# Kernel optimization log

Measured on AMD Instinct MI355X. Metric: run time of the kernel, lower is better.

The kernel has to match this reference:

```python
import jax, jax.numpy as jnp
import numpy as np

N = 80000    # total nodes
E = 640000   # total edges
B = 800      # graphs in batch
NPG = 100    # nodes per graph
HID = 128
NC = 10
IND = 20     # one-hot degree feature size (torch.eye(20))
EPS = 1e-5


def _gconv(x, src, dst, inv_out, inv_in, W, b):
    # DGL GraphConv, norm='both': D_out^{-1/2} scaling at src, sum-aggregate, D_in^{-1/2} at dst
    m = (x * inv_out[:, None])[src]                      # [E, F]
    agg = jax.ops.segment_sum(m, dst, num_segments=x.shape[0])
    return (agg * inv_in[:, None]) @ W + b


def _bn(x, gamma, beta):
    # BatchNorm1d, training-mode (batch statistics, biased variance)
    mu = x.mean(0)
    var = x.var(0)
    return (x - mu) / jnp.sqrt(var + EPS) * gamma + beta


def setup_inputs():
    key = jax.random.key(0)
    ks = jax.random.split(key, 10)
    # edges constrained within each graph (batched disjoint graphs, as in dgl.batch)
    eg = jax.random.randint(ks[0], (E,), 0, B)
    src = (eg * NPG + jax.random.randint(ks[1], (E,), 0, NPG)).astype(jnp.int32)
    dst = (eg * NPG + jax.random.randint(ks[2], (E,), 0, NPG)).astype(jnp.int32)
    graph_id = (jnp.arange(N) // NPG).astype(jnp.int32)

    def p(k, shape, fan):
        return (jax.random.normal(k, shape, jnp.float32) / np.sqrt(fan)).astype(jnp.float32)

    z = lambda s: jnp.zeros(s, jnp.float32)
    o = lambda s: jnp.ones(s, jnp.float32)
    return dict(
        src=src, dst=dst, graph_id=graph_id,
        W1=p(ks[3], (IND, HID), IND), b1=z((HID,)), g1=o((HID,)), be1=z((HID,)),
        W2=p(ks[4], (HID, HID), HID), b2=z((HID,)), g2=o((HID,)), be2=z((HID,)),
        Wv=p(ks[5], (HID, 1), HID), bv=z((1,)),
        Wd=p(ks[6], (1, HID), 1), bd=z((HID,)),
        Wg=p(ks[7], (HID, HID), HID), bg=z((HID,)), g3=o((HID,)), be3=z((HID,)),
        Wc=p(ks[8], (HID, NC), HID), bc=z((NC,)),
    )


def reference(src, dst, graph_id, W1, b1, g1, be1, W2, b2, g2, be2,
              Wv, bv, Wd, bd, Wg, bg, g3, be3, Wc, bc):
    n = graph_id.shape[0]
    ones_e = jnp.ones(src.shape[0], jnp.float32)
    in_deg = jax.ops.segment_sum(ones_e, dst, num_segments=n)
    out_deg = jax.ops.segment_sum(ones_e, src, num_segments=n)
    inv_in = jax.lax.rsqrt(jnp.maximum(in_deg, 1.0))   # DGL clamps deg min 1
    inv_out = jax.lax.rsqrt(jnp.maximum(out_deg, 1.0))

    # node features: one-hot of in-degree (eye(20)[in_degrees]); clip to valid range
    h = jax.nn.one_hot(jnp.clip(in_deg.astype(jnp.int32), 0, IND - 1), IND, dtype=jnp.float32)
    h = jax.nn.elu(_bn(_gconv(h, src, dst, inv_out, inv_in, W1, b1), g1, be1))  # [N,HID]
    h = jax.nn.elu(_bn(_gconv(h, src, dst, inv_out, inv_in, W2, b2), g2, be2))  # [N,HID]

    v = _gconv(h, src, dst, inv_out, inv_in, Wv, bv)   # [N,1], node weights d
    d = v[:, 0]

    # per-graph ragged matmul: vec_i = d_i^T @ h_i, done as one segment-sum
    vec = jax.ops.segment_sum(d[:, None] * h, graph_id, num_segments=B).reshape(-1)  # [B*HID]
    mean = vec.mean()
    vec = jax.nn.relu(vec - mean) - jax.nn.relu(-vec - mean)   # soft shrink by global mean

    hg = jnp.tanh(vec.reshape(B, HID))
    hg = jnp.tanh(_bn(hg @ Wg + bg, g3, be3))
    return jnp.tanh(hg @ Wc + bc)   # [B, NC] (eval-mode output)
```

## Files before the change

kernel.cpp:

```cpp
#include <hip/hip_runtime.h>
#include <hip/hip_bf16.h>
#include <math.h>

#define N_NODES 80000
#define N_EDGES 640000
#define B_GR 800
#define NPG 100
#define HID 128
#define NC 10
#define IND 20
#define BN_EPS 1e-5f

typedef __attribute__((ext_vector_type(8))) short bf16x8;
typedef __attribute__((ext_vector_type(4))) float f32x4;

__device__ __forceinline__ unsigned short f2bf(float f) {
    unsigned int u = __float_as_uint(f);
    u = (u + 0x7fffu + ((u >> 16) & 1u)) >> 16;
    return (unsigned short)u;
}
__device__ __forceinline__ float bf2f(unsigned short h) {
    return __uint_as_float((unsigned int)h << 16);
}

__global__ void k_A(const int* __restrict__ src, const int* __restrict__ dst,
                    unsigned int* A) {
    int e = blockIdx.x * blockDim.x + threadIdx.x;
    if (e < N_EDGES) {
        int s = src[e], d = dst[e];
        int g = d / NPG;
        int bidx = g * (NPG * NPG) + (d - g * NPG) * NPG + (s - g * NPG);
        atomicAdd(&A[bidx >> 2], 1u << ((bidx & 3) * 8));
    }
}

__global__ __launch_bounds__(128) void k_prep(const unsigned int* __restrict__ A,
                                              float* __restrict__ inv_in,
                                              float* __restrict__ inv_out,
                                              float* __restrict__ agg20) {
    __shared__ unsigned int s_A[NPG * 25];
    __shared__ float s_io[NPG];
    __shared__ int   s_ix[NPG];
    __shared__ float s_agg[NPG][IND + 1];
    int g = blockIdx.x, gbase = g * NPG, t = threadIdx.x;
    const unsigned int* Ag = A + g * 2500;
    for (int i = t; i < NPG * 25; i += 128) s_A[i] = Ag[i];
    __syncthreads();

    if (t < NPG) {
        int rsum = 0;
        const unsigned int* row = &s_A[t * 25];
#pragma unroll
        for (int q = 0; q < 25; ++q) {
            unsigned int c4 = row[q];
            rsum += (int)((c4 & 255u) + ((c4 >> 8) & 255u) + ((c4 >> 16) & 255u) + (c4 >> 24));
        }
        int csum = 0;
        int wq = t >> 2, sh = (t & 3) * 8;
#pragma unroll 4
        for (int r = 0; r < NPG; ++r)
            csum += (int)((s_A[r * 25 + wq] >> sh) & 255u);

        float io = rsqrtf(fmaxf((float)csum, 1.f));
        inv_in[gbase + t]  = rsqrtf(fmaxf((float)rsum, 1.f));
        inv_out[gbase + t] = io;
        s_io[t] = io;
        s_ix[t] = rsum > IND - 1 ? IND - 1 : rsum;
    }
    __syncthreads();

    if (t < NPG) {
#pragma unroll
        for (int k = 0; k < IND; ++k) s_agg[t][k] = 0.f;
        const unsigned int* row = &s_A[t * 25];
#pragma unroll
        for (int q = 0; q < 25; ++q) {
            unsigned int c4 = row[q];
            if (c4 == 0) continue;
#pragma unroll
            for (int b = 0; b < 4; ++b) {
                unsigned int cnt = (c4 >> (8 * b)) & 255u;
                if (cnt) {
                    int s = q * 4 + b;
                    s_agg[t][s_ix[s]] += (float)cnt * s_io[s];
                }
            }
        }
        float* outp = agg20 + (size_t)(gbase + t) * IND;
#pragma unroll
        for (int k = 0; k < IND; ++k) outp[k] = s_agg[t][k];
    }
}

#define MOM_CHUNK 64
__global__ __launch_bounds__(256) void k_mom(const float* __restrict__ agg20,
                                             const float* __restrict__ inv_in,
                                             float* s20, float* Mbuf) {
    __shared__ float rows[MOM_CHUNK * IND];
    __shared__ float w1s[MOM_CHUNK], w2s[MOM_CHUNK];
    int t = threadIdx.x;
    int k = 0, l = 0;
    bool isM = (t < 210), isS = (t >= 210 && t < 230);
    if (isM) {
        int idx = t, kk = 0;
        while (idx >= IND - kk) { idx -= IND - kk; ++kk; }
        k = kk; l = kk + idx;
    } else if (isS) {
        k = t - 210;
    }
    float acc = 0.f;
    for (int c = blockIdx.x; c < N_NODES / MOM_CHUNK; c += gridDim.x) {
        __syncthreads();
        for (int i = t * 4; i < MOM_CHUNK * IND; i += 1024)
            *(float4*)&rows[i] = *(const float4*)&agg20[(size_t)c * MOM_CHUNK * IND + i];
        if (t < MOM_CHUNK) {
            float v = inv_in[c * MOM_CHUNK + t];
            w1s[t] = v; w2s[t] = v * v;
        }
        __syncthreads();
        if (isM) {
            for (int i = 0; i < MOM_CHUNK; ++i)
                acc += w2s[i] * rows[i * IND + k] * rows[i * IND + l];
        } else if (isS) {
            for (int i = 0; i < MOM_CHUNK; ++i)
                acc += w1s[i] * rows[i * IND + k];
        }
    }
    if (isM) atomicAdd(&Mbuf[t], acc);
    else if (isS) atomicAdd(&s20[t - 210], acc);
}

__global__ void k_bn1fin(const float* __restrict__ s20, const float* __restrict__ Mbuf,
                         const float* __restrict__ W1, const float* __restrict__ b1,
                         const float* __restrict__ g1, const float* __restrict__ be1,
                         float* a1, float* c1) {
    __shared__ float sM[210], ss[IND];
    int j = threadIdx.x;
    if (j < 210) sM[j] = Mbuf[j];
    if (j + 128 < 210) sM[j + 128] = Mbuf[j + 128];
    if (j < IND) ss[j] = s20[j];
    __syncthreads();
    float w[IND];
#pragma unroll
    for (int k = 0; k < IND; ++k) w[k] = W1[k * HID + j];
    float tj = 0.f;
#pragma unroll
    for (int k = 0; k < IND; ++k) tj += ss[k] * w[k];
    float q = 0.f;
    int idx = 0;
#pragma unroll
    for (int k = 0; k < IND; ++k) {
        q += sM[idx] * w[k] * w[k]; ++idx;
#pragma unroll
        for (int l = k + 1; l < IND; ++l) { q += 2.f * sM[idx] * w[k] * w[l]; ++idx; }
    }
    float bj = b1[j];
    const float Nf = (float)N_NODES;
    float mean = (tj + Nf * bj) / Nf;
    float ey2  = (q + 2.f * bj * tj + Nf * bj * bj) / Nf;
    float var  = ey2 - mean * mean;
    float aj = g1[j] / sqrtf(var + BN_EPS);
    a1[j] = aj;
    c1[j] = be1[j] - mean * aj;
}

__global__ __launch_bounds__(256) void k_l1f(const float* __restrict__ agg20,
                                             const float* __restrict__ inv_in,
                                             const float* __restrict__ inv_out,
                                             const float* __restrict__ W1,
                                             const float* __restrict__ b1,
                                             const float* __restrict__ a1,
                                             const float* __restrict__ c1,
                                             float* __restrict__ h1s) {
    __shared__ float ws[IND * HID];
    int t = threadIdx.x;
    for (int i = t * 4; i < IND * HID; i += 1024)
        *(float4*)&ws[i] = *(const float4*)&W1[i];
    __syncthreads();
    int tx = t & 15, ty = t >> 4;
    int c0 = tx * 8;
    float4 ba = *(const float4*)(b1 + c0);
    float4 bb = *(const float4*)(b1 + c0 + 4);
    float4 aa = *(const float4*)(a1 + c0);
    float4 ab = *(const float4*)(a1 + c0 + 4);
    float4 ca = *(const float4*)(c1 + c0);
    float4 cb = *(const float4*)(c1 + c0 + 4);

    int row0 = blockIdx.x * 64 + ty * 4;
    const float* xr0 = agg20 + (size_t)row0 * IND;
    const float* xr1 = xr0 + IND;
    const float* xr2 = xr1 + IND;
    const float* xr3 = xr2 + IND;
    float acc[4][8];
#pragma unroll
    for (int r = 0; r < 4; ++r)
#pragma unroll
        for (int c = 0; c < 8; ++c) acc[r][c] = 0.f;

#pragma unroll
    for (int k = 0; k < IND; k += 4) {
        float4 x0 = *(const float4*)(xr0 + k);
        float4 x1 = *(const float4*)(xr1 + k);
        float4 x2 = *(const float4*)(xr2 + k);
        float4 x3 = *(const float4*)(xr3 + k);
#pragma unroll
        for (int kk = 0; kk < 4; ++kk) {
            float4 wa = *(const float4*)&ws[(k + kk) * HID + c0];
            float4 wb = *(const float4*)&ws[(k + kk) * HID + c0 + 4];
            float xk0 = (kk == 0) ? x0.x : (kk == 1) ? x0.y : (kk == 2) ? x0.z : x0.w;
            float xk1 = (kk == 0) ? x1.x : (kk == 1) ? x1.y : (kk == 2) ? x1.z : x1.w;
            float xk2 = (kk == 0) ? x2.x : (kk == 1) ? x2.y : (kk == 2) ? x2.z : x2.w;
            float xk3 = (kk == 0) ? x3.x : (kk == 1) ? x3.y : (kk == 2) ? x3.z : x3.w;
            acc[0][0] += xk0 * wa.x; acc[0][1] += xk0 * wa.y;
            acc[0][2] += xk0 * wa.z; acc[0][3] += xk0 * wa.w;
            acc[0][4] += xk0 * wb.x; acc[0][5] += xk0 * wb.y;
            acc[0][6] += xk0 * wb.z; acc[0][7] += xk0 * wb.w;
            acc[1][0] += xk1 * wa.x; acc[1][1] += xk1 * wa.y;
            acc[1][2] += xk1 * wa.z; acc[1][3] += xk1 * wa.w;
            acc[1][4] += xk1 * wb.x; acc[1][5] += xk1 * wb.y;
            acc[1][6] += xk1 * wb.z; acc[1][7] += xk1 * wb.w;
            acc[2][0] += xk2 * wa.x; acc[2][1] += xk2 * wa.y;
            acc[2][2] += xk2 * wa.z; acc[2][3] += xk2 * wa.w;
            acc[2][4] += xk2 * wb.x; acc[2][5] += xk2 * wb.y;
            acc[2][6] += xk2 * wb.z; acc[2][7] += xk2 * wb.w;
            acc[3][0] += xk3 * wa.x; acc[3][1] += xk3 * wa.y;
            acc[3][2] += xk3 * wa.z; acc[3][3] += xk3 * wa.w;
            acc[3][4] += xk3 * wb.x; acc[3][5] += xk3 * wb.y;
            acc[3][6] += xk3 * wb.z; acc[3][7] += xk3 * wb.w;
        }
    }
    float4 iv = *(const float4*)(inv_in + row0);
    float4 ov = *(const float4*)(inv_out + row0);
#pragma unroll
    for (int r = 0; r < 4; ++r) {
        float ivr = (r == 0) ? iv.x : (r == 1) ? iv.y : (r == 2) ? iv.z : iv.w;
        float ovr = (r == 0) ? ov.x : (r == 1) ? ov.y : (r == 2) ? ov.z : ov.w;
        float y[8];
        y[0] = acc[r][0] * ivr + ba.x; y[1] = acc[r][1] * ivr + ba.y;
        y[2] = acc[r][2] * ivr + ba.z; y[3] = acc[r][3] * ivr + ba.w;
        y[4] = acc[r][4] * ivr + bb.x; y[5] = acc[r][5] * ivr + bb.y;
        y[6] = acc[r][6] * ivr + bb.z; y[7] = acc[r][7] * ivr + bb.w;
        float z[8];
        z[0] = y[0] * aa.x + ca.x; z[1] = y[1] * aa.y + ca.y;
        z[2] = y[2] * aa.z + ca.z; z[3] = y[3] * aa.w + ca.w;
        z[4] = y[4] * ab.x + cb.x; z[5] = y[5] * ab.y + cb.y;
        z[6] = y[6] * ab.z + cb.z; z[7] = y[7] * ab.w + cb.w;
#pragma unroll
        for (int c = 0; c < 8; ++c) {
            float h = z[c] > 0.f ? z[c] : expm1f(z[c]);
            z[c] = h * ovr;
        }
        float* yr = h1s + (size_t)(row0 + r) * HID + c0;
        *(float4*)yr = make_float4(z[0], z[1], z[2], z[3]);
        *(float4*)(yr + 4) = make_float4(z[4], z[5], z[6], z[7]);
    }
}

__global__ __launch_bounds__(512) void k_agg2v5(const unsigned int* __restrict__ A,
                                                const float* __restrict__ h1s,
                                                unsigned short* __restrict__ agg2hi,
                                                unsigned short* __restrict__ agg2lo) {
    __shared__ float sh[NPG * HID];
    int t = threadIdx.x;
    int g = blockIdx.x;
    int gbase = g * NPG;

    const float4* srcp = (const float4*)(h1s + (size_t)gbase * HID);
    float4* shp = (float4*)sh;
    for (int i = t; i < (NPG * HID) / 4; i += 512)
        shp[i] = srcp[i];
    __syncthreads();

    int wv = t >> 6, lane = t & 63;
    const unsigned int* Ag = A + g * 2500;
    for (int r = wv; r < NPG; r += 8) {
        const unsigned int* row = Ag + r * 25;
        unsigned int cq[25];
#pragma unroll
        for (int q = 0; q < 25; ++q) cq[q] = row[q];
        float ax = 0.f, ay = 0.f;
#pragma unroll
        for (int q = 0; q < 25; ++q) {
            unsigned int c4 = cq[q];
            if (c4 == 0) continue;
            int sbase = q * 4;
#pragma unroll
            for (int b = 0; b < 4; ++b) {
                unsigned int cnt = (c4 >> (8 * b)) & 255u;
                if (cnt) {
                    float f = (float)cnt;
                    float2 v = *(const float2*)&sh[(sbase + b) * HID + lane * 2];
                    ax += f * v.x; ay += f * v.y;
                }
            }
        }
        unsigned short hx = f2bf(ax), hy = f2bf(ay);
        unsigned short lx = f2bf(ax - bf2f(hx)), ly = f2bf(ay - bf2f(hy));
        size_t o = (size_t)(gbase + r) * HID + lane * 2;
        *(unsigned int*)(agg2hi + o) = (unsigned int)hx | ((unsigned int)hy << 16);
        *(unsigned int*)(agg2lo + o) = (unsigned int)lx | ((unsigned int)ly << 16);
    }
}

__global__ void k_wpack(const float* __restrict__ W2, unsigned short* __restrict__ Wpack) {
    int i = blockIdx.x * 256 + threadIdx.x;
    if (i < 16384) {
        int j = i & 7, l = (i >> 3) & 63, kc = (i >> 9) & 3, nc = i >> 11;
        int k = kc * 32 + 8 * (l >> 4) + j;
        int n = nc * 16 + (l & 15);
        float w = W2[k * HID + n];
        unsigned short h = f2bf(w);
        Wpack[i] = h;
        Wpack[16384 + i] = f2bf(w - bf2f(h));
    }
}

__global__ __launch_bounds__(512) void k_l2mf(const unsigned short* __restrict__ agg2hi,
                                              const unsigned short* __restrict__ agg2lo,
                                              const float* __restrict__ inv_in,
                                              const unsigned short* __restrict__ Wpack,
                                              const float* __restrict__ b2,
                                              float* __restrict__ y2,
                                              float* sums, float* sqs) {
    __shared__ unsigned short wp[32768];
    int t = threadIdx.x;
    for (int i = t; i < 4096; i += 512)
        ((bf16x8*)wp)[i] = ((const bf16x8*)Wpack)[i];
    __syncthreads();

    int w = t >> 6, l = t & 63;
    int lg = l >> 4, lr = l & 15;
    int row0 = blockIdx.x * 128 + w * 16;

    bf16x8 ah[4], al[4];
    const unsigned short* ahb = agg2hi + (size_t)(row0 + lr) * HID;
    const unsigned short* alb = agg2lo + (size_t)(row0 + lr) * HID;
#pragma unroll
    for (int kc = 0; kc < 4; ++kc) {
        ah[kc] = *(const bf16x8*)(ahb + kc * 32 + 8 * lg);
        al[kc] = *(const bf16x8*)(alb + kc * 32 + 8 * lg);
    }

    f32x4 acc[8];
#pragma unroll
    for (int nc = 0; nc < 8; ++nc) acc[nc] = (f32x4)(0.f);
#pragma unroll
    for (int nc = 0; nc < 8; ++nc) {
#pragma unroll
        for (int kc = 0; kc < 4; ++kc) {
            const unsigned short* bp = wp + ((nc * 4 + kc) * 64 + l) * 8;
            bf16x8 bh = *(const bf16x8*)bp;
            bf16x8 bl = *(const bf16x8*)(bp + 16384);
            acc[nc] = __builtin_amdgcn_mfma_f32_16x16x32_bf16(ah[kc], bh, acc[nc], 0, 0, 0);
            acc[nc] = __builtin_amdgcn_mfma_f32_16x16x32_bf16(ah[kc], bl, acc[nc], 0, 0, 0);
            acc[nc] = __builtin_amdgcn_mfma_f32_16x16x32_bf16(al[kc], bh, acc[nc], 0, 0, 0);
        }
    }

    float iv[4];
#pragma unroll
    for (int r = 0; r < 4; ++r) iv[r] = inv_in[row0 + 4 * lg + r];
    float ys[8][4];
#pragma unroll
    for (int nc = 0; nc < 8; ++nc) {
        int col = nc * 16 + lr;
        float bj = b2[col];
#pragma unroll
        for (int r = 0; r < 4; ++r) {
            float y = acc[nc][r] * iv[r] + bj;
            ys[nc][r] = y;
            y2[(size_t)(row0 + 4 * lg + r) * HID + col] = y;
        }
    }

    __syncthreads();
    float* red = (float*)wp;
    if (t < 256) red[t] = 0.f;
    __syncthreads();
#pragma unroll
    for (int nc = 0; nc < 8; ++nc) {
        int col = nc * 16 + lr;
        float cs = ys[nc][0] + ys[nc][1] + ys[nc][2] + ys[nc][3];
        float cq = ys[nc][0] * ys[nc][0] + ys[nc][1] * ys[nc][1]
                 + ys[nc][2] * ys[nc][2] + ys[nc][3] * ys[nc][3];
        atomicAdd(&red[col], cs);
        atomicAdd(&red[128 + col], cq);
    }
    __syncthreads();
    if (t < HID) {
        atomicAdd(&sums[t], red[t]);
        atomicAdd(&sqs[t], red[128 + t]);
    }
}

__global__ void k_bnfin(const float* sums, const float* sqs,
                        const float* gamma, const float* beta,
                        float cnt, float* a, float* c) {
    int j = threadIdx.x;
    float mu  = sums[j] / cnt;
    float var = sqs[j] / cnt - mu * mu;
    float aj  = gamma[j] / sqrtf(var + BN_EPS);
    a[j] = aj;
    c[j] = beta[j] - mu * aj;
}

__global__ __launch_bounds__(512) void k_post(const unsigned int* __restrict__ A,
                                              const float* __restrict__ y2,
                                              const float* __restrict__ a2,
                                              const float* __restrict__ c2,
                                              const float* __restrict__ inv_in,
                                              const float* __restrict__ inv_out,
                                              const float* __restrict__ Wv,
                                              const float* __restrict__ bv,
                                              float* __restrict__ vec,
                                              float* meansum) {
    __shared__ float sh[NPG * HID];
    __shared__ float s_p[NPG];
    __shared__ float s_d[NPG];
    __shared__ float s_red[512];
    int t = threadIdx.x;
    int g = blockIdx.x, gbase = g * NPG;

    const float4* srcp = (const float4*)(y2 + (size_t)gbase * HID);
    for (int i = t; i < (NPG * HID) / 4; i += 512) {
        int col = (i * 4) & (HID - 1);
        float4 v = srcp[i];
        float4 av = *(const float4*)(a2 + col);
        float4 cv = *(const float4*)(c2 + col);
        float z0 = v.x * av.x + cv.x; z0 = z0 > 0.f ? z0 : expm1f(z0);
        float z1 = v.y * av.y + cv.y; z1 = z1 > 0.f ? z1 : expm1f(z1);
        float z2 = v.z * av.z + cv.z; z2 = z2 > 0.f ? z2 : expm1f(z2);
        float z3 = v.w * av.w + cv.w; z3 = z3 > 0.f ? z3 : expm1f(z3);
        *(float4*)&sh[i * 4] = make_float4(z0, z1, z2, z3);
    }
    __syncthreads();

    int wv = t >> 6, lane = t & 63;
    float2 wvv = *(const float2*)(Wv + lane * 2);
    for (int r = wv; r < NPG; r += 8) {
        float2 h = *(const float2*)&sh[r * HID + lane * 2];
        float d = h.x * wvv.x + h.y * wvv.y;
        for (int off = 32; off; off >>= 1) d += __shfl_down(d, off);
        if (lane == 0) s_p[r] = d * inv_out[gbase + r];
    }
    __syncthreads();

    if (t < NPG) {
        const unsigned int* row = A + g * 2500 + t * 25;
        unsigned int cq[25];
#pragma unroll
        for (int q = 0; q < 25; ++q) cq[q] = row[q];
        float acc = 0.f;
#pragma unroll
        for (int q = 0; q < 25; ++q) {
            unsigned int c4 = cq[q];
            if (c4 == 0) continue;
#pragma unroll
            for (int b = 0; b < 4; ++b) {
                unsigned int cnt = (c4 >> (8 * b)) & 255u;
                if (cnt) acc += (float)cnt * s_p[q * 4 + b];
            }
        }
        s_d[t] = acc * inv_in[gbase + t] + bv[0];
    }
    __syncthreads();

    int col = t & (HID - 1);
    int qr = t >> 7;
    float part = 0.f;
    for (int r = qr * 25; r < qr * 25 + 25; ++r)
        part += s_d[r] * sh[r * HID + col];
    s_red[qr * HID + col] = part;
    __syncthreads();
    if (t < HID) {
        float v = s_red[t] + s_red[HID + t] + s_red[2 * HID + t] + s_red[3 * HID + t];
        vec[g * HID + t] = v;
        for (int off = 32; off; off >>= 1) v += __shfl_down(v, off);
        if ((t & 63) == 0) atomicAdd(meansum, v);
    }
}

__global__ __launch_bounds__(128) void k_g1(const float* __restrict__ vec,
                                            const float* __restrict__ meansum,
                                            const float* __restrict__ Wg,
                                            const float* __restrict__ bg,
                                            float* y3, float* sums, float* sqs) {
    __shared__ float ws[HID * HID];
    __shared__ float rows[HID];
    int g = blockIdx.x, j = threadIdx.x;
    for (int k = 0; k < HID; ++k) ws[k * HID + j] = Wg[k * HID + j];
    float mean = meansum[0] * (1.f / (B_GR * HID));
    float v = vec[g * HID + j];
    float sh = fmaxf(v - mean, 0.f) - fmaxf(-v - mean, 0.f);
    rows[j] = tanhf(sh);
    __syncthreads();
    float acc = 0.f;
#pragma unroll 8
    for (int k = 0; k < HID; ++k) acc += rows[k] * ws[k * HID + j];
    float y = acc + bg[j];
    y3[g * HID + j] = y;
    atomicAdd(&sums[j], y);
    atomicAdd(&sqs[j], y * y);
}

__global__ __launch_bounds__(128) void k_out(const float* __restrict__ y3,
                                             const float* __restrict__ a,
                                             const float* __restrict__ c,
                                             const float* __restrict__ Wc,
                                             const float* __restrict__ bc,
                                             float* out) {
    __shared__ float hg[HID];
    int g = blockIdx.x, j = threadIdx.x;
    hg[j] = tanhf(y3[g * HID + j] * a[j] + c[j]);
    __syncthreads();
    if (j < NC) {
        float acc = 0.f;
        for (int k = 0; k < HID; ++k) acc += hg[k] * Wc[k * NC + j];
        out[g * NC + j] = tanhf(acc + bc[j]);
    }
}

extern "C" void kernel_launch(void* const* d_in, const int* in_sizes, int n_in,
                              void* d_out, int out_size, void* d_ws, size_t ws_size,
                              hipStream_t stream) {
    const int*   src = (const int*)d_in[0];
    const int*   dst = (const int*)d_in[1];
    const float* W1  = (const float*)d_in[3];
    const float* b1  = (const float*)d_in[4];
    const float* g1  = (const float*)d_in[5];
    const float* be1 = (const float*)d_in[6];
    const float* W2  = (const float*)d_in[7];
    const float* b2  = (const float*)d_in[8];
    const float* g2  = (const float*)d_in[9];
    const float* be2 = (const float*)d_in[10];
    const float* Wv  = (const float*)d_in[11];
    const float* bv  = (const float*)d_in[12];
    const float* Wg  = (const float*)d_in[15];
    const float* bg  = (const float*)d_in[16];
    const float* g3  = (const float*)d_in[17];
    const float* be3 = (const float*)d_in[18];
    const float* Wc  = (const float*)d_in[19];
    const float* bc  = (const float*)d_in[20];
    float* out = (float*)d_out;

    char* ws = (char*)d_ws;
    size_t off = 0;
    auto carve = [&](size_t bytes) -> char* {
        char* pp = ws + off;
        off = (off + bytes + 255) & ~(size_t)255;
        return pp;
    };
    unsigned int* A = (unsigned int*)carve((size_t)B_GR * NPG * NPG);
    float* stats   = (float*)carve(2048 * 4);
    size_t zbytes = off;
    float* inv_in  = (float*)carve(N_NODES * 4);
    float* inv_out = (float*)carve(N_NODES * 4);
    float* vec     = (float*)carve((size_t)B_GR * HID * 4);
    float* y3      = (float*)carve((size_t)B_GR * HID * 4);
    float* agg20   = (float*)carve((size_t)N_NODES * IND * 4);
    float* bufA    = (float*)carve((size_t)N_NODES * HID * 4);
    unsigned short* agg2hi = (unsigned short*)carve((size_t)N_NODES * HID * 2);
    unsigned short* agg2lo = (unsigned short*)carve((size_t)N_NODES * HID * 2);
    unsigned short* Wpack  = (unsigned short*)carve(32768 * 2);

    float* sums2 = stats + 0;    float* sq2 = stats + 128;
    float* a2    = stats + 256;  float* c2  = stats + 384;
    float* sums3 = stats + 512;  float* sq3 = stats + 640;
    float* a3    = stats + 768;  float* c3  = stats + 896;
    float* meansum = stats + 1024;
    float* s20   = stats + 1056;
    float* Mbuf  = stats + 1088;
    float* a1    = stats + 1312;
    float* c1    = stats + 1440;

    hipMemsetAsync(d_ws, 0, zbytes, stream);

    k_A<<<(N_EDGES + 255) / 256, 256, 0, stream>>>(src, dst, A);
    k_wpack<<<64, 256, 0, stream>>>(W2, Wpack);
    k_prep<<<B_GR, 128, 0, stream>>>(A, inv_in, inv_out, agg20);
    k_mom<<<320, 256, 0, stream>>>(agg20, inv_in, s20, Mbuf);
    k_bn1fin<<<1, 128, 0, stream>>>(s20, Mbuf, W1, b1, g1, be1, a1, c1);
    k_l1f<<<N_NODES / 64, 256, 0, stream>>>(agg20, inv_in, inv_out, W1, b1, a1, c1, bufA);
    k_agg2v5<<<B_GR, 512, 0, stream>>>(A, bufA, agg2hi, agg2lo);
    k_l2mf<<<N_NODES / 128, 512, 0, stream>>>(agg2hi, agg2lo, inv_in, Wpack, b2,
                                              bufA, sums2, sq2);
    k_bnfin<<<1, 128, 0, stream>>>(sums2, sq2, g2, be2, (float)N_NODES, a2, c2);
    k_post<<<B_GR, 512, 0, stream>>>(A, bufA, a2, c2, inv_in, inv_out, Wv, bv, vec, meansum);
    k_g1<<<B_GR, 128, 0, stream>>>(vec, meansum, Wg, bg, y3, sums3, sq3);
    k_bnfin<<<1, 128, 0, stream>>>(sums3, sq3, g3, be3, (float)B_GR, a3, c3);
    k_out<<<B_GR, 128, 0, stream>>>(y3, a3, c3, Wc, bc, out);
}
```

Before: 292.2 us.

## Build per-graph sparse CSR edge lists and split layer-2 MFMA tiles by column half

k_prep now prefix-sums the nonzeros of each row of the per-graph dense count matrix and writes a compact CSR-style list (source index plus count) with per-row offsets. k_agg2 and k_post walk these lists instead of scanning 25 packed words per row with branches. Separately, k_l2mf is split into column halves with 64-row tiles and 256 threads, halving its LDS weight footprint and doubling the block count. The costs are extra writes in k_prep, a scan with several barriers, and a fixed per-graph capacity of 1024 entries that overflows if a graph has more unique edges.

```diff
diff --git a/kernel.cpp b/kernel.cpp
--- a/kernel.cpp
+++ b/kernel.cpp
@@ -10,6 +10,7 @@
 #define NC 10
 #define IND 20
 #define BN_EPS 1e-5f
+#define ENT_CAP 1024
 
 typedef __attribute__((ext_vector_type(8))) short bf16x8;
 typedef __attribute__((ext_vector_type(4))) float f32x4;
@@ -37,16 +38,20 @@
 __global__ __launch_bounds__(128) void k_prep(const unsigned int* __restrict__ A,
                                               float* __restrict__ inv_in,
                                               float* __restrict__ inv_out,
-                                              float* __restrict__ agg20) {
+                                              float* __restrict__ agg20,
+                                              unsigned int* __restrict__ ent,
+                                              int* __restrict__ goff) {
     __shared__ unsigned int s_A[NPG * 25];
     __shared__ float s_io[NPG];
     __shared__ int   s_ix[NPG];
     __shared__ float s_agg[NPG][IND + 1];
+    __shared__ int s_offs[128];
     int g = blockIdx.x, gbase = g * NPG, t = threadIdx.x;
     const unsigned int* Ag = A + g * 2500;
     for (int i = t; i < NPG * 25; i += 128) s_A[i] = Ag[i];
     __syncthreads();
 
+    int nnz = 0;
     if (t < NPG) {
         int rsum = 0;
         const unsigned int* row = &s_A[t * 25];
@@ -54,6 +59,8 @@
         for (int q = 0; q < 25; ++q) {
             unsigned int c4 = row[q];
             rsum += (int)((c4 & 255u) + ((c4 >> 8) & 255u) + ((c4 >> 16) & 255u) + (c4 >> 24));
+            nnz += (int)((c4 & 255u) != 0) + (int)(((c4 >> 8) & 255u) != 0)
+                 + (int)(((c4 >> 16) & 255u) != 0) + (int)((c4 >> 24) != 0);
         }
         int csum = 0;
         int wq = t >> 2, sh = (t & 3) * 8;
@@ -67,12 +74,26 @@
         s_io[t] = io;
         s_ix[t] = rsum > IND - 1 ? IND - 1 : rsum;
     }
+    int v = nnz;
+    s_offs[t] = v;
+    __syncthreads();
+    for (int d = 1; d < 128; d <<= 1) {
+        int x = (t >= d) ? s_offs[t - d] : 0;
+        __syncthreads();
+        s_offs[t] += x;
+        __syncthreads();
+    }
+    int my_off = s_offs[t] - v;
+    if (t < NPG) goff[g * 104 + t] = my_off;
+    if (t == 0) goff[g * 104 + NPG] = s_offs[127];
     __syncthreads();
 
     if (t < NPG) {
 #pragma unroll
         for (int k = 0; k < IND; ++k) s_agg[t][k] = 0.f;
         const unsigned int* row = &s_A[t * 25];
+        unsigned int* ep = ent + (size_t)g * ENT_CAP + my_off;
+        int w = 0;
 #pragma unroll
         for (int q = 0; q < 25; ++q) {
             unsigned int c4 = row[q];
@@ -83,6 +104,7 @@
                 if (cnt) {
                     int s = q * 4 + b;
                     s_agg[t][s_ix[s]] += (float)cnt * s_io[s];
+                    ep[w++] = ((unsigned int)s << 8) | cnt;
                 }
             }
         }
@@ -256,11 +278,13 @@
     }
 }
 
-__global__ __launch_bounds__(512) void k_agg2v5(const unsigned int* __restrict__ A,
+__global__ __launch_bounds__(512) void k_agg2v6(const unsigned int* __restrict__ ent,
+                                                const int* __restrict__ goff,
                                                 const float* __restrict__ h1s,
                                                 unsigned short* __restrict__ agg2hi,
                                                 unsigned short* __restrict__ agg2lo) {
     __shared__ float sh[NPG * HID];
+    __shared__ int s_off[NPG + 1];
     int t = threadIdx.x;
     int g = blockIdx.x;
     int gbase = g * NPG;
@@ -269,30 +293,33 @@
     float4* shp = (float4*)sh;
     for (int i = t; i < (NPG * HID) / 4; i += 512)
         shp[i] = srcp[i];
+    if (t <= NPG) s_off[t] = goff[g * 104 + t];
     __syncthreads();
 
     int wv = t >> 6, lane = t & 63;
-    const unsigned int* Ag = A + g * 2500;
+    const unsigned int* ep = ent + (size_t)g * ENT_CAP;
     for (int r = wv; r < NPG; r += 8) {
-        const unsigned int* row = Ag + r * 25;
-        unsigned int cq[25];
-#pragma unroll
-        for (int q = 0; q < 25; ++q) cq[q] = row[q];
+        int e0 = s_off[r], e1 = s_off[r + 1];
         float ax = 0.f, ay = 0.f;
-#pragma unroll
-        for (int q = 0; q < 25; ++q) {
-            unsigned int c4 = cq[q];
-            if (c4 == 0) continue;
-            int sbase = q * 4;
-#pragma unroll
-            for (int b = 0; b < 4; ++b) {
-                unsigned int cnt = (c4 >> (8 * b)) & 255u;
-                if (cnt) {
-                    float f = (float)cnt;
-                    float2 v = *(const float2*)&sh[(sbase + b) * HID + lane * 2];
-                    ax += f * v.x; ay += f * v.y;
-                }
+        int i = e0;
+        for (; i + 8 <= e1; i += 8) {
+            unsigned int ee[8];
+#pragma unroll
+            for (int j = 0; j < 8; ++j) ee[j] = ep[i + j];
+#pragma unroll
+            for (int j = 0; j < 8; ++j) {
+                float f = (float)(ee[j] & 255u);
+                int s = ee[j] >> 8;
+                float2 v = *(const float2*)&sh[s * HID + lane * 2];
+                ax += f * v.x; ay += f * v.y;
             }
+        }
+        for (; i < e1; ++i) {
+            unsigned int e = ep[i];
+            float f = (float)(e & 255u);
+            int s = e >> 8;
+            float2 v = *(const float2*)&sh[s * HID + lane * 2];
+            ax += f * v.x; ay += f * v.y;
         }
         unsigned short hx = f2bf(ax), hy = f2bf(ay);
         unsigned short lx = f2bf(ax - bf2f(hx)), ly = f2bf(ay - bf2f(hy));
@@ -315,22 +342,28 @@
     }
 }
 
-__global__ __launch_bounds__(512) void k_l2mf(const unsigned short* __restrict__ agg2hi,
+__global__ __launch_bounds__(256) void k_l2mf(const unsigned short* __restrict__ agg2hi,
                                               const unsigned short* __restrict__ agg2lo,
                                               const float* __restrict__ inv_in,
                                               const unsigned short* __restrict__ Wpack,
                                               const float* __restrict__ b2,
                                               float* __restrict__ y2,
                                               float* sums, float* sqs) {
-    __shared__ unsigned short wp[32768];
+    __shared__ unsigned short wp[16384];
     int t = threadIdx.x;
-    for (int i = t; i < 4096; i += 512)
-        ((bf16x8*)wp)[i] = ((const bf16x8*)Wpack)[i];
+    int tile = blockIdx.x >> 1, half = blockIdx.x & 1;
+    int cbase = half * 64;
+    const bf16x8* ghi = (const bf16x8*)(Wpack + half * 8192);
+    const bf16x8* glo = (const bf16x8*)(Wpack + 16384 + half * 8192);
+    for (int i = t; i < 1024; i += 256) {
+        ((bf16x8*)wp)[i] = ghi[i];
+        ((bf16x8*)(wp + 8192))[i] = glo[i];
+    }
     __syncthreads();
 
     int w = t >> 6, l = t & 63;
     int lg = l >> 4, lr = l & 15;
-    int row0 = blockIdx.x * 128 + w * 16;
+    int row0 = tile * 64 + w * 16;
 
     bf16x8 ah[4], al[4];
     const unsigned short* ahb = agg2hi + (size_t)(row0 + lr) * HID;
@@ -341,55 +374,55 @@
         al[kc] = *(const bf16x8*)(alb + kc * 32 + 8 * lg);
     }
 
-    f32x4 acc[8];
-#pragma unroll
-    for (int nc = 0; nc < 8; ++nc) acc[nc] = (f32x4)(0.f);
-#pragma unroll
-    for (int nc = 0; nc < 8; ++nc) {
+    f32x4 acc[4];
+#pragma unroll
+    for (int ncl = 0; ncl < 4; ++ncl) acc[ncl] = (f32x4)(0.f);
+#pragma unroll
+    for (int ncl = 0; ncl < 4; ++ncl) {
 #pragma unroll
         for (int kc = 0; kc < 4; ++kc) {
-            const unsigned short* bp = wp + ((nc * 4 + kc) * 64 + l) * 8;
+            const unsigned short* bp = wp + ((ncl * 4 + kc) * 64 + l) * 8;
             bf16x8 bh = *(const bf16x8*)bp;
-            bf16x8 bl = *(const bf16x8*)(bp + 16384);
-            acc[nc] = __builtin_amdgcn_mfma_f32_16x16x32_bf16(ah[kc], bh, acc[nc], 0, 0, 0);
-            acc[nc] = __builtin_amdgcn_mfma_f32_16x16x32_bf16(ah[kc], bl, acc[nc], 0, 0, 0);
-            acc[nc] = __builtin_amdgcn_mfma_f32_16x16x32_bf16(al[kc], bh, acc[nc], 0, 0, 0);
+            bf16x8 bl = *(const bf16x8*)(bp + 8192);
+            acc[ncl] = __builtin_amdgcn_mfma_f32_16x16x32_bf16(ah[kc], bh, acc[ncl], 0, 0, 0);
+            acc[ncl] = __builtin_amdgcn_mfma_f32_16x16x32_bf16(ah[kc], bl, acc[ncl], 0, 0, 0);
+            acc[ncl] = __builtin_amdgcn_mfma_f32_16x16x32_bf16(al[kc], bh, acc[ncl], 0, 0, 0);
         }
     }
 
     float iv[4];
 #pragma unroll
     for (int r = 0; r < 4; ++r) iv[r] = inv_in[row0 + 4 * lg + r];
-    float ys[8][4];
-#pragma unroll
-    for (int nc = 0; nc < 8; ++nc) {
-        int col = nc * 16 + lr;
+    float ys[4][4];
+#pragma unroll
+    for (int ncl = 0; ncl < 4; ++ncl) {
+        int col = cbase + ncl * 16 + lr;
         float bj = b2[col];
 #pragma unroll
         for (int r = 0; r < 4; ++r) {
-            float y = acc[nc][r] * iv[r] + bj;
-            ys[nc][r] = y;
+            float y = acc[ncl][r] * iv[r] + bj;
+            ys[ncl][r] = y;
             y2[(size_t)(row0 + 4 * lg + r) * HID + col] = y;
         }
     }
 
     __syncthreads();
     float* red = (float*)wp;
-    if (t < 256) red[t] = 0.f;
-    __syncthreads();
-#pragma unroll
-    for (int nc = 0; nc < 8; ++nc) {
-        int col = nc * 16 + lr;
-        float cs = ys[nc][0] + ys[nc][1] + ys[nc][2] + ys[nc][3];
-        float cq = ys[nc][0] * ys[nc][0] + ys[nc][1] * ys[nc][1]
-                 + ys[nc][2] * ys[nc][2] + ys[nc][3] * ys[nc][3];
-        atomicAdd(&red[col], cs);
-        atomicAdd(&red[128 + col], cq);
-    }
-    __syncthreads();
-    if (t < HID) {
-        atomicAdd(&sums[t], red[t]);
-        atomicAdd(&sqs[t], red[128 + t]);
+    if (t < 128) red[t] = 0.f;
+    __syncthreads();
+#pragma unroll
+    for (int ncl = 0; ncl < 4; ++ncl) {
+        int lcol = ncl * 16 + lr;
+        float cs = ys[ncl][0] + ys[ncl][1] + ys[ncl][2] + ys[ncl][3];
+        float cq = ys[ncl][0] * ys[ncl][0] + ys[ncl][1] * ys[ncl][1]
+                 + ys[ncl][2] * ys[ncl][2] + ys[ncl][3] * ys[ncl][3];
+        atomicAdd(&red[lcol], cs);
+        atomicAdd(&red[64 + lcol], cq);
+    }
+    __syncthreads();
+    if (t < 64) {
+        atomicAdd(&sums[cbase + t], red[t]);
+        atomicAdd(&sqs[cbase + t], red[64 + t]);
     }
 }
 
@@ -404,7 +437,8 @@
     c[j] = beta[j] - mu * aj;
 }
 
-__global__ __launch_bounds__(512) void k_post(const unsigned int* __restrict__ A,
+__global__ __launch_bounds__(512) void k_post(const unsigned int* __restrict__ ent,
+                                              const int* __restrict__ goff,
                                               const float* __restrict__ y2,
                                               const float* __restrict__ a2,
                                               const float* __restrict__ c2,
@@ -418,6 +452,7 @@
     __shared__ float s_p[NPG];
     __shared__ float s_d[NPG];
     __shared__ float s_red[512];
+    __shared__ int s_off[NPG + 1];
     int t = threadIdx.x;
     int g = blockIdx.x, gbase = g * NPG;
 
@@ -433,6 +468,7 @@
         float z3 = v.w * av.w + cv.w; z3 = z3 > 0.f ? z3 : expm1f(z3);
         *(float4*)&sh[i * 4] = make_float4(z0, z1, z2, z3);
     }
+    if (t <= NPG) s_off[t] = goff[g * 104 + t];
     __syncthreads();
 
     int wv = t >> 6, lane = t & 63;
@@ -446,20 +482,12 @@
     __syncthreads();
 
     if (t < NPG) {
-        const unsigned int* row = A + g * 2500 + t * 25;
-        unsigned int cq[25];
-#pragma unroll
-        for (int q = 0; q < 25; ++q) cq[q] = row[q];
+        const unsigned int* ep = ent + (size_t)g * ENT_CAP;
+        int e0 = s_off[t], e1 = s_off[t + 1];
         float acc = 0.f;
-#pragma unroll
-        for (int q = 0; q < 25; ++q) {
-            unsigned int c4 = cq[q];
-            if (c4 == 0) continue;
-#pragma unroll
-            for (int b = 0; b < 4; ++b) {
-                unsigned int cnt = (c4 >> (8 * b)) & 255u;
-                if (cnt) acc += (float)cnt * s_p[q * 4 + b];
-            }
+        for (int i = e0; i < e1; ++i) {
+            unsigned int e = ep[i];
+            acc += (float)(e & 255u) * s_p[e >> 8];
         }
         s_d[t] = acc * inv_in[gbase + t] + bv[0];
     }
@@ -562,6 +590,8 @@
     unsigned short* agg2hi = (unsigned short*)carve((size_t)N_NODES * HID * 2);
     unsigned short* agg2lo = (unsigned short*)carve((size_t)N_NODES * HID * 2);
     unsigned short* Wpack  = (unsigned short*)carve(32768 * 2);
+    unsigned int* ent = (unsigned int*)carve((size_t)B_GR * ENT_CAP * 4);
+    int* goff      = (int*)carve((size_t)B_GR * 104 * 4);
 
     float* sums2 = stats + 0;    float* sq2 = stats + 128;
     float* a2    = stats + 256;  float* c2  = stats + 384;
@@ -577,15 +607,16 @@
 
     k_A<<<(N_EDGES + 255) / 256, 256, 0, stream>>>(src, dst, A);
     k_wpack<<<64, 256, 0, stream>>>(W2, Wpack);
-    k_prep<<<B_GR, 128, 0, stream>>>(A, inv_in, inv_out, agg20);
+    k_prep<<<B_GR, 128, 0, stream>>>(A, inv_in, inv_out, agg20, ent, goff);
     k_mom<<<320, 256, 0, stream>>>(agg20, inv_in, s20, Mbuf);
     k_bn1fin<<<1, 128, 0, stream>>>(s20, Mbuf, W1, b1, g1, be1, a1, c1);
     k_l1f<<<N_NODES / 64, 256, 0, stream>>>(agg20, inv_in, inv_out, W1, b1, a1, c1, bufA);
-    k_agg2v5<<<B_GR, 512, 0, stream>>>(A, bufA, agg2hi, agg2lo);
-    k_l2mf<<<N_NODES / 128, 512, 0, stream>>>(agg2hi, agg2lo, inv_in, Wpack, b2,
-                                              bufA, sums2, sq2);
+    k_agg2v6<<<B_GR, 512, 0, stream>>>(ent, goff, bufA, agg2hi, agg2lo);
+    k_l2mf<<<(N_NODES / 64) * 2, 256, 0, stream>>>(agg2hi, agg2lo, inv_in, Wpack, b2,
+                                                   bufA, sums2, sq2);
     k_bnfin<<<1, 128, 0, stream>>>(sums2, sq2, g2, be2, (float)N_NODES, a2, c2);
-    k_post<<<B_GR, 512, 0, stream>>>(A, bufA, a2, c2, inv_in, inv_out, Wv, bv, vec, meansum);
+    k_post<<<B_GR, 512, 0, stream>>>(ent, goff, bufA, a2, c2, inv_in, inv_out, Wv, bv,
+                                     vec, meansum);
     k_g1<<<B_GR, 128, 0, stream>>>(vec, meansum, Wg, bg, y3, sums3, sq3);
     k_bnfin<<<1, 128, 0, stream>>>(sums3, sq3, g3, be3, (float)B_GR, a3, c3);
     k_out<<<B_GR, 128, 0, stream>>>(y3, a3, c3, Wc, bc, out);
```

After: 276.7 us. -5.3%, faster.
